# Performance work log

Hardware: AMD Instinct MI355X
Metric: run time of the kernel (lower is better)

Reference implementation:

```python
import jax, jax.numpy as jnp
import numpy as np

D_MODEL = 2048
FFN_MULT = 4
N_ROUTED = 8
TOP_K = 2
H_ROUTED = FFN_MULT * D_MODEL // N_ROUTED   # 1024
H_SHARED = FFN_MULT * D_MODEL               # 8192


def setup_inputs() -> dict:
    key = jax.random.key(0)
    ks = jax.random.split(key, 8)
    s = 0.02
    x = jax.random.normal(ks[0], (4, 2048, D_MODEL), dtype=jnp.float32)
    w_gate = jax.random.normal(ks[1], (N_ROUTED, D_MODEL), dtype=jnp.float32) * s
    Wg = jax.random.normal(ks[2], (N_ROUTED, D_MODEL, H_ROUTED), dtype=jnp.float32) * s
    Wu = jax.random.normal(ks[3], (N_ROUTED, D_MODEL, H_ROUTED), dtype=jnp.float32) * s
    Wd = jax.random.normal(ks[4], (N_ROUTED, H_ROUTED, D_MODEL), dtype=jnp.float32) * s
    Sg = jax.random.normal(ks[5], (D_MODEL, H_SHARED), dtype=jnp.float32) * s
    Su = jax.random.normal(ks[6], (D_MODEL, H_SHARED), dtype=jnp.float32) * s
    Sd = jax.random.normal(ks[7], (H_SHARED, D_MODEL), dtype=jnp.float32) * s
    return {"x": x, "w_gate": w_gate, "Wg": Wg, "Wu": Wu, "Wd": Wd,
            "Sg": Sg, "Su": Su, "Sd": Sd}


def reference(x, w_gate, Wg, Wu, Wd, Sg, Su, Sd):
    B, T, D = x.shape
    N = B * T
    xf = x.reshape(N, D)

    # shared expert (n_shared = 1)
    shared = (jax.nn.silu(xf @ Sg) * (xf @ Su)) @ Sd          # [N, D]

    # gate (eval mode: clean logits, no noise)
    clean = xf @ w_gate.T                                      # [N, E]
    top_logits, top_idx = jax.lax.top_k(clean, TOP_K)          # [N, K]
    gates = jax.nn.softmax(top_logits, axis=-1)                # [N, K]
    # load-balance loss
    importance = jax.nn.softmax(clean, axis=-1).sum(0)         # [E]
    ce = importance / N * N_ROUTED
    lb_loss = jnp.mean(ce * ce)

    # combine weights: combine[n,e] = sum_k gates[n,k] * (top_idx[n,k]==e)
    onehot = jax.nn.one_hot(top_idx, N_ROUTED, dtype=xf.dtype)  # [N, K, E]
    combine = jnp.einsum('nke,nk->ne', onehot, gates)           # [N, E]

    # routed experts (dense grouped form, zero-weight tokens contribute 0)
    hg = jnp.einsum('nd,edh->neh', xf, Wg)
    hu = jnp.einsum('nd,edh->neh', xf, Wu)
    h = jax.nn.silu(hg) * hu                                    # [N, E, H]
    routed = jnp.einsum('neh,ehd,ne->nd', h, Wd, combine)       # [N, D]

    out = (shared + routed).reshape(B, T, D)
    return out, lb_loss
```

## Files before the change

kernel.cpp:

```cpp
#include <hip/hip_runtime.h>
#include <hip/hip_bf16.h>
#include <hip/hip_fp16.h>
#include <stdint.h>

#define NTOK   8192
#define DM     2048
#define NEXP   8
#define HR     1024
#define HS     8192
#define ROWS_MAX 18432

typedef _Float16 f16;
typedef f16  f16x8 __attribute__((ext_vector_type(8)));
typedef float f32x4 __attribute__((ext_vector_type(4)));

#define GLP(p) ((const __attribute__((address_space(1))) void*)(p))
#define LDP(p) ((__attribute__((address_space(3))) void*)(p))

static __device__ __forceinline__ float silu_f(float v) {
  return v / (1.0f + __expf(-v));
}

static __device__ __forceinline__ int xcd_swz(int bid, int nwg) {
  const int q = nwg >> 3, r = nwg & 7;
  const int x = bid & 7, i = bid >> 3;
  return (x < r ? x * (q + 1) : r * (q + 1) + (x - r) * q) + i;
}


__global__ __launch_bounds__(256)
void conv_x_kernel(const float* __restrict__ in, f16* __restrict__ out, int n8) {
  const int i = blockIdx.x * 256 + threadIdx.x;
  if (i >= n8) return;
  const float4* p = (const float4*)in + (size_t)i * 2;
  const float4 a = p[0], b = p[1];
  f16x8 o;
  o[0] = (f16)a.x; o[1] = (f16)a.y; o[2] = (f16)a.z; o[3] = (f16)a.w;
  o[4] = (f16)b.x; o[5] = (f16)b.y; o[6] = (f16)b.z; o[7] = (f16)b.w;
  ((f16x8*)out)[i] = o;
}

__global__ __launch_bounds__(256)
void conv_t_kernel(const float* __restrict__ in, f16* __restrict__ out,
                   int R, int C, size_t ostride, int rmap) {
  __shared__ float t[32][33];
  const int b = blockIdx.z;
  const float* inb = in + (size_t)b * R * C;
  f16* outb = out + (size_t)b * ostride;
  const int c0 = blockIdx.x * 32, r0 = blockIdx.y * 32;
  const int tx = threadIdx.x, ty0 = threadIdx.y;
#pragma unroll
  for (int yy = 0; yy < 4; ++yy) {
    const int ty = ty0 + yy * 8;
    t[ty][tx] = inb[(size_t)(r0 + ty) * C + (c0 + tx)];
  }
  __syncthreads();
#pragma unroll
  for (int yy = 0; yy < 4; ++yy) {
    const int ty = ty0 + yy * 8;
    const int tr = c0 + ty;
    const int pr = rmap ? (((tr >> 4) << 5) + ((rmap - 1) << 4) + (tr & 15)) : tr;
    outb[(size_t)pr * R + (r0 + tx)] = (f16)t[tx][ty];
  }
}


__global__ __launch_bounds__(256)
void gate_kernel(const float* __restrict__ x, const float* __restrict__ wgate,
                 float* __restrict__ gateW, int* __restrict__ gateI,
                 float* __restrict__ importance, int* __restrict__ cnt) {
  __shared__ float impl[NEXP];
  __shared__ int cntl[NEXP];
  const int tid = threadIdx.x, lane = tid & 63, wid = tid >> 6;
  if (tid < NEXP) { impl[tid] = 0.f; cntl[tid] = 0; }
  __syncthreads();
  for (int s = 0; s < 8; ++s) {
    const int t = blockIdx.x * 32 + wid * 8 + s;
    const float* xr = x + (size_t)t * DM;
    float pv[NEXP] = {0.f, 0.f, 0.f, 0.f, 0.f, 0.f, 0.f, 0.f};
    for (int j = 0; j < DM / 64; ++j) {
      const int c = lane + j * 64;
      const float xv = xr[c];
#pragma unroll
      for (int e = 0; e < NEXP; ++e) pv[e] += xv * wgate[e * DM + c];
    }
#pragma unroll
    for (int e = 0; e < NEXP; ++e) {
#pragma unroll
      for (int st = 32; st >= 1; st >>= 1) pv[e] += __shfl_xor(pv[e], st);
    }
    if (lane == 0) {
      float v1 = pv[0]; int i1 = 0;
#pragma unroll
      for (int e = 1; e < NEXP; ++e) if (pv[e] > v1) { v1 = pv[e]; i1 = e; }
      float v2 = -1e30f; int i2 = 0;
#pragma unroll
      for (int e = 0; e < NEXP; ++e) if (e != i1 && pv[e] > v2) { v2 = pv[e]; i2 = e; }
      const float g1 = 1.f / (1.f + expf(v2 - v1));
      gateW[t * 2 + 0] = g1;  gateW[t * 2 + 1] = 1.f - g1;
      gateI[t * 2 + 0] = i1;  gateI[t * 2 + 1] = i2;
      float mx = pv[0];
#pragma unroll
      for (int e = 1; e < NEXP; ++e) mx = fmaxf(mx, pv[e]);
      float sum = 0.f, ex[NEXP];
#pragma unroll
      for (int e = 0; e < NEXP; ++e) { ex[e] = expf(pv[e] - mx); sum += ex[e]; }
      const float inv = 1.f / sum;
#pragma unroll
      for (int e = 0; e < NEXP; ++e) atomicAdd(&impl[e], ex[e] * inv);
      atomicAdd(&cntl[i1], 1);
      atomicAdd(&cntl[i2], 1);
    }
  }
  __syncthreads();
  if (tid < NEXP) {
    atomicAdd(&importance[tid], impl[tid]);
    atomicAdd(&cnt[tid], cntl[tid]);
  }
}

__global__ void scan_kernel(const int* __restrict__ cnt, int* __restrict__ seg,
                            int* __restrict__ cursor, const float* __restrict__ imp,
                            float* __restrict__ lb_out) {
  if (threadIdx.x == 0 && blockIdx.x == 0) {
    int o = 0;
#pragma unroll
    for (int e = 0; e < NEXP; ++e) {
      seg[e] = o;
      o += (cnt[e] + 255) & ~255;
      cursor[e] = 0;
    }
    seg[NEXP] = o;
    float s = 0.f;
#pragma unroll
    for (int e = 0; e < NEXP; ++e) {
      const float ce = imp[e] * ((float)NEXP / (float)NTOK);
      s += ce * ce;
    }
    *lb_out = s / (float)NEXP;
  }
}

__global__ __launch_bounds__(256)
void scatter_kernel(const float* __restrict__ gateW, const int* __restrict__ gateI,
                    const int* __restrict__ seg, int* __restrict__ cursor,
                    int* __restrict__ rowtok, float* __restrict__ rowgate) {
  const int t = blockIdx.x * 256 + threadIdx.x;
  const int lane = threadIdx.x & 63;
#pragma unroll
  for (int k = 0; k < 2; ++k) {
    const int e = gateI[t * 2 + k];
    const float g = gateW[t * 2 + k];
    for (int ee = 0; ee < NEXP; ++ee) {
      const unsigned long long m = __ballot(e == ee);
      if (e == ee) {
        const int leader = __ffsll((unsigned long long)m) - 1;
        const int rank = (int)__popcll(m & ((1ull << lane) - 1ull));
        int base = 0;
        if (lane == leader) base = atomicAdd(&cursor[ee], (int)__popcll(m));
        base = __shfl(base, leader);
        const int pos = seg[ee] + base + rank;
        rowtok[pos] = t;
        rowgate[pos] = g;
      }
    }
  }
}


struct G8Ptrs { const f16* a[4]; const f16* b[4]; };

static __device__ __forceinline__ void swz_rc(int tid, int i, int& r, int& c) {
  const int L = i * 8192 + tid * 16;
  const int U = L ^ (((L >> 7) & 7) << 4);
  r = U >> 7;
  c = (U & 127) >> 1;
}

static __device__ __forceinline__ void stage8(const G8Ptrs& P, int koff,
                                              f16* AsB, f16* BsB, int wid) {
#pragma unroll
  for (int i = 0; i < 4; ++i) {
    __builtin_amdgcn_global_load_lds(GLP(P.a[i] + koff), LDP(AsB + i * 4096 + wid * 512), 16, 0, 0);
    __builtin_amdgcn_global_load_lds(GLP(P.b[i] + koff), LDP(BsB + i * 4096 + wid * 512), 16, 0, 0);
  }
}

static __device__ __forceinline__ void g8_mainloop(const G8Ptrs& P, int nt,
                                                   f16* As, f16* Bs,
                                                   f32x4 (&acc)[8][4]) {
  const int tid = threadIdx.x;
  const int lane = tid & 63, wid = tid >> 6;
  const int wr = wid >> 2, wc = wid & 3;
  const int fr = lane & 15, fk = (lane >> 4) * 8;

  stage8(P, 0, As, Bs, wid);
  asm volatile("s_waitcnt vmcnt(0)" ::: "memory");
  __syncthreads();

  for (int t = 0; t < nt; ++t) {
    const int cur = t & 1;
    if (t + 1 < nt)
      stage8(P, (t + 1) * 64, As + (cur ^ 1) * 16384, Bs + (cur ^ 1) * 16384, wid);
    const f16* Ab = As + cur * 16384;
    const f16* Bb = Bs + cur * 16384;
    f16x8 bf[4][2];
#pragma unroll
    for (int n = 0; n < 4; ++n) {
      const int r = wc * 64 + n * 16 + fr;
      const int sw = (r & 7) << 3;
#pragma unroll
      for (int ks = 0; ks < 2; ++ks)
        bf[n][ks] = *(const f16x8*)&Bb[(r * 64 + ks * 32 + fk) ^ sw];
    }
#pragma unroll
    for (int mh = 0; mh < 2; ++mh) {
#pragma unroll
      for (int ks = 0; ks < 2; ++ks) {
        f16x8 af[4];
#pragma unroll
        for (int m = 0; m < 4; ++m) {
          const int r = wr * 128 + (mh * 4 + m) * 16 + fr;
          af[m] = *(const f16x8*)&Ab[(r * 64 + ks * 32 + fk) ^ ((r & 7) << 3)];
        }
#pragma unroll
        for (int m = 0; m < 4; ++m)
#pragma unroll
          for (int n = 0; n < 4; ++n)
            acc[mh * 4 + m][n] =
                __builtin_amdgcn_mfma_f32_16x16x32_f16(af[m], bf[n][ks], acc[mh * 4 + m][n], 0, 0, 0);
      }
    }
    asm volatile("s_waitcnt vmcnt(0)" ::: "memory");
    __syncthreads();
  }
}

__global__ __launch_bounds__(512, 2)
void g8_gu(const f16* __restrict__ A, const f16* __restrict__ B,
           f16* __restrict__ H, int gx, int Nh, int K) {
  __shared__ f16 As[2 * 16384], Bs[2 * 16384];
  const int lin = xcd_swz(blockIdx.x, gridDim.x);
  const int row0 = (lin % gx) * 256, n0 = (lin / gx) * 256;
  const int tid = threadIdx.x;
  G8Ptrs P;
#pragma unroll
  for (int i = 0; i < 4; ++i) {
    int r, c; swz_rc(tid, i, r, c);
    P.a[i] = A + (size_t)(row0 + r) * K + c;
    P.b[i] = B + (size_t)(n0 + r) * K + c;
  }
  f32x4 acc[8][4] = {};
  g8_mainloop(P, K / 64, As, Bs, acc);
  const int lane = tid & 63, wid = tid >> 6;
  const int wr = wid >> 2, wc = wid & 3;
  const int fr = lane & 15, r0 = (lane >> 4) * 4;
  const int hc0 = (n0 + wc * 64) >> 1;
#pragma unroll
  for (int m = 0; m < 8; ++m)
#pragma unroll
    for (int k = 0; k < 2; ++k)
#pragma unroll
      for (int rr = 0; rr < 4; ++rr) {
        const int row = row0 + wr * 128 + m * 16 + r0 + rr;
        const int hcol = hc0 + k * 16 + fr;
        const float g = acc[m][2 * k][rr];
        const float u = acc[m][2 * k + 1][rr];
        H[(size_t)row * Nh + hcol] = (f16)(silu_f(g) * u);
      }
}

__global__ __launch_bounds__(512, 2)
void g8_down(const f16* __restrict__ A, const f16* __restrict__ B,
             float* __restrict__ out, int gx, int N, int K) {
  __shared__ f16 As[2 * 16384], Bs[2 * 16384];
  const int lin = xcd_swz(blockIdx.x, gridDim.x);
  const int row0 = (lin % gx) * 256, n0 = (lin / gx) * 256;
  const int tid = threadIdx.x;
  G8Ptrs P;
#pragma unroll
  for (int i = 0; i < 4; ++i) {
    int r, c; swz_rc(tid, i, r, c);
    P.a[i] = A + (size_t)(row0 + r) * K + c;
    P.b[i] = B + (size_t)(n0 + r) * K + c;
  }
  f32x4 acc[8][4] = {};
  g8_mainloop(P, K / 64, As, Bs, acc);
  const int lane = tid & 63, wid = tid >> 6;
  const int wr = wid >> 2, wc = wid & 3;
  const int fr = lane & 15, r0 = (lane >> 4) * 4;
#pragma unroll
  for (int m = 0; m < 8; ++m)
#pragma unroll
    for (int n = 0; n < 4; ++n)
#pragma unroll
      for (int rr = 0; rr < 4; ++rr) {
        const int row = row0 + wr * 128 + m * 16 + r0 + rr;
        const int col = n0 + wc * 64 + n * 16 + fr;
        out[(size_t)row * N + col] = acc[m][n][rr];
      }
}

__global__ __launch_bounds__(512, 2)
void g8_rgu(const f16* __restrict__ x16, const int* __restrict__ rowtok,
            const f16* __restrict__ Wgu, f16* __restrict__ hr,
            const int* __restrict__ seg) {
  __shared__ f16 As[2 * 16384], Bs[2 * 16384];
  const int e = blockIdx.z;
  const int row0 = seg[e] + blockIdx.y * 256;
  if (row0 >= seg[e + 1]) return;
  const int n0 = blockIdx.x * 256;
  const f16* Bbase = Wgu + (size_t)e * 2048 * DM;
  const int tid = threadIdx.x;
  G8Ptrs P;
#pragma unroll
  for (int i = 0; i < 4; ++i) {
    int r, c; swz_rc(tid, i, r, c);
    int tok = rowtok[row0 + r];
    if (tok < 0) tok = 0;
    P.a[i] = x16 + (size_t)tok * DM + c;
    P.b[i] = Bbase + (size_t)(n0 + r) * DM + c;
  }
  f32x4 acc[8][4] = {};
  g8_mainloop(P, DM / 64, As, Bs, acc);
  const int lane = tid & 63, wid = tid >> 6;
  const int wr = wid >> 2, wc = wid & 3;
  const int fr = lane & 15, r0 = (lane >> 4) * 4;
  const int hc0 = (n0 + wc * 64) >> 1;
#pragma unroll
  for (int m = 0; m < 8; ++m)
#pragma unroll
    for (int k = 0; k < 2; ++k)
#pragma unroll
      for (int rr = 0; rr < 4; ++rr) {
        const int row = row0 + wr * 128 + m * 16 + r0 + rr;
        const int hcol = hc0 + k * 16 + fr;
        const float g = acc[m][2 * k][rr];
        const float u = acc[m][2 * k + 1][rr];
        hr[(size_t)row * HR + hcol] = (f16)(silu_f(g) * u);
      }
}

__global__ __launch_bounds__(512, 2)
void g8_rdown(const f16* __restrict__ A, const f16* __restrict__ B,
              float* __restrict__ out, const int* __restrict__ seg,
              const int* __restrict__ rowtok, const float* __restrict__ rowgate) {
  __shared__ f16 As[2 * 16384], Bs[2 * 16384];
  const int e = blockIdx.z;
  const int row0 = seg[e] + blockIdx.y * 256;
  if (row0 >= seg[e + 1]) return;
  const int n0 = blockIdx.x * 256;
  const f16* Bbase = B + (size_t)e * DM * HR;
  const int tid = threadIdx.x;
  G8Ptrs P;
#pragma unroll
  for (int i = 0; i < 4; ++i) {
    int r, c; swz_rc(tid, i, r, c);
    P.a[i] = A + (size_t)(row0 + r) * HR + c;
    P.b[i] = Bbase + (size_t)(n0 + r) * HR + c;
  }
  f32x4 acc[8][4] = {};
  g8_mainloop(P, HR / 64, As, Bs, acc);
  const int lane = tid & 63, wid = tid >> 6;
  const int wr = wid >> 2, wc = wid & 3;
  const int fr = lane & 15, r0 = (lane >> 4) * 4;
#pragma unroll
  for (int m = 0; m < 8; ++m)
#pragma unroll
    for (int rr = 0; rr < 4; ++rr) {
      const int pos = row0 + wr * 128 + m * 16 + r0 + rr;
      const int tok = rowtok[pos];
      if (tok >= 0) {
        const float gw = rowgate[pos];
#pragma unroll
        for (int n = 0; n < 4; ++n) {
          const int col = n0 + wc * 64 + n * 16 + fr;
          atomicAdd(&out[(size_t)tok * DM + col], acc[m][n][rr] * gw);
        }
      }
    }
}


extern "C" void kernel_launch(void* const* d_in, const int* in_sizes, int n_in,
                              void* d_out, int out_size, void* d_ws, size_t ws_size,
                              hipStream_t stream) {
  const float* x  = (const float*)d_in[0];
  const float* wg = (const float*)d_in[1];
  const float* Wg = (const float*)d_in[2];
  const float* Wu = (const float*)d_in[3];
  const float* Wd = (const float*)d_in[4];
  const float* Sg = (const float*)d_in[5];
  const float* Su = (const float*)d_in[6];
  const float* Sd = (const float*)d_in[7];
  float* out = (float*)d_out;

  char* p = (char*)d_ws;
  auto take = [&](size_t b) { char* q = p; p += (b + 255) & ~(size_t)255; return q; };
  float* importance = (float*)take(32);
  int*   cnt        = (int*)take(32);
  int*   cursor     = (int*)take(32);
  int*   seg        = (int*)take(64);
  int*   rowtok     = (int*)take((size_t)ROWS_MAX * 4);
  float* rowgate    = (float*)take((size_t)ROWS_MAX * 4);
  float* gateW      = (float*)take((size_t)NTOK * 2 * 4);
  int*   gateI      = (int*)take((size_t)NTOK * 2 * 4);
  f16* x16   = (f16*)take((size_t)NTOK * DM * 2);
  f16* SguI  = (f16*)take((size_t)2 * HS * DM * 2);
  f16* SdT   = (f16*)take((size_t)DM * HS * 2);
  f16* WguI  = (f16*)take((size_t)NEXP * 2048 * DM * 2);
  f16* WdT   = (f16*)take((size_t)NEXP * DM * HR * 2);
  f16* hbuf  = (f16*)take((size_t)NTOK * HS * 2);
  f16* hr    = (f16*)take((size_t)ROWS_MAX * HR * 2);
  if ((size_t)(p - (char*)d_ws) > ws_size) return;

  hipMemsetAsync(importance, 0, 768, stream);
  hipMemsetAsync(rowtok, 0xFF, (size_t)ROWS_MAX * 4, stream);

  conv_x_kernel<<<(NTOK * DM / 8 + 255) / 256, 256, 0, stream>>>(x, x16, NTOK * DM / 8);
  dim3 tb(32, 8);
  conv_t_kernel<<<dim3(HS / 32, DM / 32, 1), tb, 0, stream>>>(Sg, SguI, DM, HS, 0, 1);
  conv_t_kernel<<<dim3(HS / 32, DM / 32, 1), tb, 0, stream>>>(Su, SguI, DM, HS, 0, 2);
  conv_t_kernel<<<dim3(DM / 32, HS / 32, 1), tb, 0, stream>>>(Sd, SdT, HS, DM, 0, 0);
  conv_t_kernel<<<dim3(HR / 32, DM / 32, NEXP), tb, 0, stream>>>(Wg, WguI, DM, HR, (size_t)2048 * DM, 1);
  conv_t_kernel<<<dim3(HR / 32, DM / 32, NEXP), tb, 0, stream>>>(Wu, WguI, DM, HR, (size_t)2048 * DM, 2);
  conv_t_kernel<<<dim3(DM / 32, HR / 32, NEXP), tb, 0, stream>>>(Wd, WdT, HR, DM, (size_t)DM * HR, 0);

  gate_kernel<<<NTOK / 32, 256, 0, stream>>>(x, wg, gateW, gateI, importance, cnt);
  scan_kernel<<<1, 64, 0, stream>>>(cnt, seg, cursor, importance, out + (size_t)NTOK * DM);
  scatter_kernel<<<NTOK / 256, 256, 0, stream>>>(gateW, gateI, seg, cursor, rowtok, rowgate);

  g8_rgu<<<dim3(8, 64, NEXP), 512, 0, stream>>>(x16, rowtok, WguI, hr, seg);

  g8_gu<<<32 * 64, 512, 0, stream>>>(x16, SguI, hbuf, 32, HS, DM);
  g8_down<<<32 * 8, 512, 0, stream>>>(hbuf, SdT, out, 32, DM, HS);

  g8_rdown<<<dim3(8, 64, NEXP), 512, 0, stream>>>(hr, WdT, out, seg, rowtok, rowgate);
}
```

Baseline: 1.447 ms.

## Split GEMM mainloop into half-tile phases with finer prefetch waits; pre-gather routed rows

The shared GEMM mainloop now issues next-tile LDS prefetches in two halves around two barriers. It waits with partial vmcnt counts so the second half of the A tile loads while the first half of the MFMAs runs, rather than waiting for all loads at the end of each iteration. A new gather kernel copies routed token rows into a contiguous buffer (aliased onto hbuf, which is only written later), so the routed gate/up GEMM reads contiguous rows instead of indirecting through rowtok. This adds an extra memory pass and a launch. The hand-tuned waitcnt counts must exactly match the number of outstanding loads for correctness.

Measured after the change: 1.881 ms. 30.0% more time.

```diff
diff --git a/kernel.cpp b/kernel.cpp
--- a/kernel.cpp
+++ b/kernel.cpp
@@ -167,6 +167,19 @@
   }
 }
 
+__global__ __launch_bounds__(256)
+void gather_kernel(const f16* __restrict__ x16, const int* __restrict__ rowtok,
+                   f16* __restrict__ xg) {
+  const int row = blockIdx.x * 4 + (threadIdx.x >> 6);
+  const int lane = threadIdx.x & 63;
+  int tok = rowtok[row];
+  if (tok < 0) tok = 0;
+  const uint4* src = (const uint4*)(x16 + (size_t)tok * DM);
+  uint4* dst = (uint4*)(xg + (size_t)row * DM);
+#pragma unroll
+  for (int i = 0; i < 4; ++i) dst[lane + i * 64] = src[lane + i * 64];
+}
+
 
 struct G8Ptrs { const f16* a[4]; const f16* b[4]; };
 
@@ -175,15 +188,6 @@
   const int U = L ^ (((L >> 7) & 7) << 4);
   r = U >> 7;
   c = (U & 127) >> 1;
-}
-
-static __device__ __forceinline__ void stage8(const G8Ptrs& P, int koff,
-                                              f16* AsB, f16* BsB, int wid) {
-#pragma unroll
-  for (int i = 0; i < 4; ++i) {
-    __builtin_amdgcn_global_load_lds(GLP(P.a[i] + koff), LDP(AsB + i * 4096 + wid * 512), 16, 0, 0);
-    __builtin_amdgcn_global_load_lds(GLP(P.b[i] + koff), LDP(BsB + i * 4096 + wid * 512), 16, 0, 0);
-  }
 }
 
 static __device__ __forceinline__ void g8_mainloop(const G8Ptrs& P, int nt,
@@ -194,46 +198,76 @@
   const int wr = wid >> 2, wc = wid & 3;
   const int fr = lane & 15, fk = (lane >> 4) * 8;
 
-  stage8(P, 0, As, Bs, wid);
-  asm volatile("s_waitcnt vmcnt(0)" ::: "memory");
-  __syncthreads();
+#define STG_A(BUF, KOFF, U) \
+  __builtin_amdgcn_global_load_lds(GLP(P.a[U] + (KOFF)), LDP((BUF) + (U) * 4096 + wid * 512), 16, 0, 0)
+#define STG_B(BUF, KOFF, U) \
+  __builtin_amdgcn_global_load_lds(GLP(P.b[U] + (KOFF)), LDP((BUF) + (U) * 4096 + wid * 512), 16, 0, 0)
+
+  STG_B(Bs, 0, 0); STG_B(Bs, 0, 1); STG_B(Bs, 0, 2); STG_B(Bs, 0, 3);
+  STG_A(As, 0, 0); STG_A(As, 0, 2);
+  STG_A(As, 0, 1); STG_A(As, 0, 3);
 
   for (int t = 0; t < nt; ++t) {
     const int cur = t & 1;
-    if (t + 1 < nt)
-      stage8(P, (t + 1) * 64, As + (cur ^ 1) * 16384, Bs + (cur ^ 1) * 16384, wid);
     const f16* Ab = As + cur * 16384;
     const f16* Bb = Bs + cur * 16384;
+    f16* An = As + (cur ^ 1) * 16384;
+    f16* Bn = Bs + (cur ^ 1) * 16384;
+    const int koff = (t + 1) * 64;
+    const bool pf = (t + 1 < nt);
+
+    asm volatile("s_waitcnt vmcnt(2) lgkmcnt(0)" ::: "memory");
+    __builtin_amdgcn_s_barrier();
+    if (pf) {
+      STG_B(Bn, koff, 0); STG_B(Bn, koff, 1); STG_B(Bn, koff, 2); STG_B(Bn, koff, 3);
+      STG_A(An, koff, 0); STG_A(An, koff, 2);
+    }
     f16x8 bf[4][2];
 #pragma unroll
     for (int n = 0; n < 4; ++n) {
       const int r = wc * 64 + n * 16 + fr;
       const int sw = (r & 7) << 3;
-#pragma unroll
-      for (int ks = 0; ks < 2; ++ks)
-        bf[n][ks] = *(const f16x8*)&Bb[(r * 64 + ks * 32 + fk) ^ sw];
-    }
-#pragma unroll
-    for (int mh = 0; mh < 2; ++mh) {
-#pragma unroll
-      for (int ks = 0; ks < 2; ++ks) {
-        f16x8 af[4];
-#pragma unroll
-        for (int m = 0; m < 4; ++m) {
-          const int r = wr * 128 + (mh * 4 + m) * 16 + fr;
-          af[m] = *(const f16x8*)&Ab[(r * 64 + ks * 32 + fk) ^ ((r & 7) << 3)];
-        }
-#pragma unroll
-        for (int m = 0; m < 4; ++m)
-#pragma unroll
-          for (int n = 0; n < 4; ++n)
-            acc[mh * 4 + m][n] =
-                __builtin_amdgcn_mfma_f32_16x16x32_f16(af[m], bf[n][ks], acc[mh * 4 + m][n], 0, 0, 0);
-      }
-    }
-    asm volatile("s_waitcnt vmcnt(0)" ::: "memory");
-    __syncthreads();
-  }
+      bf[n][0] = *(const f16x8*)&Bb[(r * 64 + fk) ^ sw];
+      bf[n][1] = *(const f16x8*)&Bb[(r * 64 + 32 + fk) ^ sw];
+    }
+#pragma unroll
+    for (int ks = 0; ks < 2; ++ks) {
+      f16x8 af[4];
+#pragma unroll
+      for (int m = 0; m < 4; ++m) {
+        const int r = wr * 128 + m * 16 + fr;
+        af[m] = *(const f16x8*)&Ab[(r * 64 + ks * 32 + fk) ^ ((r & 7) << 3)];
+      }
+#pragma unroll
+      for (int m = 0; m < 4; ++m)
+#pragma unroll
+        for (int n = 0; n < 4; ++n)
+          acc[m][n] = __builtin_amdgcn_mfma_f32_16x16x32_f16(af[m], bf[n][ks], acc[m][n], 0, 0, 0);
+    }
+    if (pf) {
+      asm volatile("s_waitcnt vmcnt(6) lgkmcnt(0)" ::: "memory");
+    } else {
+      asm volatile("s_waitcnt vmcnt(0) lgkmcnt(0)" ::: "memory");
+    }
+    __builtin_amdgcn_s_barrier();
+    if (pf) { STG_A(An, koff, 1); STG_A(An, koff, 3); }
+#pragma unroll
+    for (int ks = 0; ks < 2; ++ks) {
+      f16x8 af[4];
+#pragma unroll
+      for (int m = 0; m < 4; ++m) {
+        const int r = wr * 128 + (4 + m) * 16 + fr;
+        af[m] = *(const f16x8*)&Ab[(r * 64 + ks * 32 + fk) ^ ((r & 7) << 3)];
+      }
+#pragma unroll
+      for (int m = 0; m < 4; ++m)
+#pragma unroll
+        for (int n = 0; n < 4; ++n)
+          acc[4 + m][n] = __builtin_amdgcn_mfma_f32_16x16x32_f16(af[m], bf[n][ks], acc[4 + m][n], 0, 0, 0);
+    }
+  }
+#undef STG_A
+#undef STG_B
 }
 
 __global__ __launch_bounds__(512, 2)
@@ -302,9 +336,8 @@
 }
 
 __global__ __launch_bounds__(512, 2)
-void g8_rgu(const f16* __restrict__ x16, const int* __restrict__ rowtok,
-            const f16* __restrict__ Wgu, f16* __restrict__ hr,
-            const int* __restrict__ seg) {
+void g8_rgu(const f16* __restrict__ xg, const f16* __restrict__ Wgu,
+            f16* __restrict__ hr, const int* __restrict__ seg) {
   __shared__ f16 As[2 * 16384], Bs[2 * 16384];
   const int e = blockIdx.z;
   const int row0 = seg[e] + blockIdx.y * 256;
@@ -316,9 +349,7 @@
 #pragma unroll
   for (int i = 0; i < 4; ++i) {
     int r, c; swz_rc(tid, i, r, c);
-    int tok = rowtok[row0 + r];
-    if (tok < 0) tok = 0;
-    P.a[i] = x16 + (size_t)tok * DM + c;
+    P.a[i] = xg + (size_t)(row0 + r) * DM + c;
     P.b[i] = Bbase + (size_t)(n0 + r) * DM + c;
   }
   f32x4 acc[8][4] = {};
@@ -412,6 +443,7 @@
   f16* WdT   = (f16*)take((size_t)NEXP * DM * HR * 2);
   f16* hbuf  = (f16*)take((size_t)NTOK * HS * 2);
   f16* hr    = (f16*)take((size_t)ROWS_MAX * HR * 2);
+  f16* xg    = hbuf;
   if ((size_t)(p - (char*)d_ws) > ws_size) return;
 
   hipMemsetAsync(importance, 0, 768, stream);
@@ -429,8 +461,9 @@
   gate_kernel<<<NTOK / 32, 256, 0, stream>>>(x, wg, gateW, gateI, importance, cnt);
   scan_kernel<<<1, 64, 0, stream>>>(cnt, seg, cursor, importance, out + (size_t)NTOK * DM);
   scatter_kernel<<<NTOK / 256, 256, 0, stream>>>(gateW, gateI, seg, cursor, rowtok, rowgate);
-
-  g8_rgu<<<dim3(8, 64, NEXP), 512, 0, stream>>>(x16, rowtok, WguI, hr, seg);
+  gather_kernel<<<ROWS_MAX / 4, 256, 0, stream>>>(x16, rowtok, xg);
+
+  g8_rgu<<<dim3(8, 64, NEXP), 512, 0, stream>>>(xg, WguI, hr, seg);
 
   g8_gu<<<32 * 64, 512, 0, stream>>>(x16, SguI, hbuf, 32, HS, DM);
   g8_down<<<32 * 8, 512, 0, stream>>>(hbuf, SdT, out, 32, DM, HS);
```

## Merge shared and routed expert GEMMs into single combined launches

Applied to the files above, without the earlier changes.

Folds the routed gate/up GEMM into the shared gate/up launch and the routed down GEMM into the shared down launch. Routed blocks are indexed over flattened row tiles, and each block finds its expert with a lookup over the segment offsets. The point is to fill the GPU better: the shared down GEMM alone launches only 256 large blocks, so routed work can run beside it, and the tails of the separate launches overlap. In exchange, the shared down output must now be written with atomic adds into an output buffer zeroed by an added memset, which costs extra memory traffic and atomic overhead.

Result: slower. 1.685 ms (+16.5%).

```diff
diff --git a/kernel.cpp b/kernel.cpp
--- a/kernel.cpp
+++ b/kernel.cpp
@@ -9,6 +9,7 @@
 #define HR     1024
 #define HS     8192
 #define ROWS_MAX 18432
+#define YT_MAX 72
 
 typedef _Float16 f16;
 typedef f16  f16x8 __attribute__((ext_vector_type(8)));
@@ -236,25 +237,56 @@
   }
 }
 
+static __device__ __forceinline__ int seg_lookup(const int* __restrict__ seg, int r0) {
+  int e = 0;
+#pragma unroll
+  for (int k = 1; k < NEXP; ++k) if (r0 >= seg[k]) e = k;
+  return e;
+}
+
 __global__ __launch_bounds__(512, 2)
-void g8_gu(const f16* __restrict__ A, const f16* __restrict__ B,
-           f16* __restrict__ H, int gx, int Nh, int K) {
+void g8_gu_all(const f16* __restrict__ x16, const f16* __restrict__ SguI,
+               f16* __restrict__ hbuf, const f16* __restrict__ Wgu,
+               f16* __restrict__ hr, const int* __restrict__ rowtok,
+               const int* __restrict__ seg) {
   __shared__ f16 As[2 * 16384], Bs[2 * 16384];
-  const int lin = xcd_swz(blockIdx.x, gridDim.x);
-  const int row0 = (lin % gx) * 256, n0 = (lin / gx) * 256;
   const int tid = threadIdx.x;
   G8Ptrs P;
-#pragma unroll
-  for (int i = 0; i < 4; ++i) {
-    int r, c; swz_rc(tid, i, r, c);
-    P.a[i] = A + (size_t)(row0 + r) * K + c;
-    P.b[i] = B + (size_t)(n0 + r) * K + c;
+  f16* H;
+  int Nh, row0, n0;
+  if (blockIdx.x < 2048) {
+    const int lin = xcd_swz(blockIdx.x, 2048);
+    row0 = (lin & 31) * 256;
+    n0 = (lin >> 5) * 256;
+#pragma unroll
+    for (int i = 0; i < 4; ++i) {
+      int r, c; swz_rc(tid, i, r, c);
+      P.a[i] = x16 + (size_t)(row0 + r) * DM + c;
+      P.b[i] = SguI + (size_t)(n0 + r) * DM + c;
+    }
+    H = hbuf; Nh = HS;
+  } else {
+    const int rb = blockIdx.x - 2048;
+    n0 = (rb & 7) * 256;
+    row0 = (rb >> 3) * 256;
+    if (row0 >= seg[NEXP]) return;
+    const int e = seg_lookup(seg, row0);
+    const f16* Bbase = Wgu + (size_t)e * 2048 * DM;
+#pragma unroll
+    for (int i = 0; i < 4; ++i) {
+      int r, c; swz_rc(tid, i, r, c);
+      int tok = rowtok[row0 + r];
+      if (tok < 0) tok = 0;
+      P.a[i] = x16 + (size_t)tok * DM + c;
+      P.b[i] = Bbase + (size_t)(n0 + r) * DM + c;
+    }
+    H = hr; Nh = HR;
   }
   f32x4 acc[8][4] = {};
-  g8_mainloop(P, K / 64, As, Bs, acc);
+  g8_mainloop(P, DM / 64, As, Bs, acc);
   const int lane = tid & 63, wid = tid >> 6;
   const int wr = wid >> 2, wc = wid & 3;
-  const int fr = lane & 15, r0 = (lane >> 4) * 4;
+  const int fr = lane & 15, r0v = (lane >> 4) * 4;
   const int hc0 = (n0 + wc * 64) >> 1;
 #pragma unroll
   for (int m = 0; m < 8; ++m)
@@ -262,7 +294,7 @@
     for (int k = 0; k < 2; ++k)
 #pragma unroll
       for (int rr = 0; rr < 4; ++rr) {
-        const int row = row0 + wr * 128 + m * 16 + r0 + rr;
+        const int row = row0 + wr * 128 + m * 16 + r0v + rr;
         const int hcol = hc0 + k * 16 + fr;
         const float g = acc[m][2 * k][rr];
         const float u = acc[m][2 * k + 1][rr];
@@ -271,114 +303,74 @@
 }
 
 __global__ __launch_bounds__(512, 2)
-void g8_down(const f16* __restrict__ A, const f16* __restrict__ B,
-             float* __restrict__ out, int gx, int N, int K) {
+void g8_down_all(const f16* __restrict__ hbuf, const f16* __restrict__ SdT,
+                 const f16* __restrict__ hr, const f16* __restrict__ WdT,
+                 float* __restrict__ out, const int* __restrict__ seg,
+                 const int* __restrict__ rowtok, const float* __restrict__ rowgate) {
   __shared__ f16 As[2 * 16384], Bs[2 * 16384];
-  const int lin = xcd_swz(blockIdx.x, gridDim.x);
-  const int row0 = (lin % gx) * 256, n0 = (lin / gx) * 256;
   const int tid = threadIdx.x;
   G8Ptrs P;
-#pragma unroll
-  for (int i = 0; i < 4; ++i) {
-    int r, c; swz_rc(tid, i, r, c);
-    P.a[i] = A + (size_t)(row0 + r) * K + c;
-    P.b[i] = B + (size_t)(n0 + r) * K + c;
+  int row0, n0, nt;
+  bool routed;
+  if (blockIdx.x < 256) {
+    const int lin = xcd_swz(blockIdx.x, 256);
+    row0 = (lin & 31) * 256;
+    n0 = (lin >> 5) * 256;
+#pragma unroll
+    for (int i = 0; i < 4; ++i) {
+      int r, c; swz_rc(tid, i, r, c);
+      P.a[i] = hbuf + (size_t)(row0 + r) * HS + c;
+      P.b[i] = SdT + (size_t)(n0 + r) * HS + c;
+    }
+    nt = HS / 64; routed = false;
+  } else {
+    const int rb = blockIdx.x - 256;
+    n0 = (rb & 7) * 256;
+    row0 = (rb >> 3) * 256;
+    if (row0 >= seg[NEXP]) return;
+    const int e = seg_lookup(seg, row0);
+    const f16* Bbase = WdT + (size_t)e * DM * HR;
+#pragma unroll
+    for (int i = 0; i < 4; ++i) {
+      int r, c; swz_rc(tid, i, r, c);
+      P.a[i] = hr + (size_t)(row0 + r) * HR + c;
+      P.b[i] = Bbase + (size_t)(n0 + r) * HR + c;
+    }
+    nt = HR / 64; routed = true;
   }
   f32x4 acc[8][4] = {};
-  g8_mainloop(P, K / 64, As, Bs, acc);
+  g8_mainloop(P, nt, As, Bs, acc);
   const int lane = tid & 63, wid = tid >> 6;
   const int wr = wid >> 2, wc = wid & 3;
-  const int fr = lane & 15, r0 = (lane >> 4) * 4;
-#pragma unroll
-  for (int m = 0; m < 8; ++m)
-#pragma unroll
-    for (int n = 0; n < 4; ++n)
+  const int fr = lane & 15, r0v = (lane >> 4) * 4;
+  if (!routed) {
+#pragma unroll
+    for (int m = 0; m < 8; ++m)
+#pragma unroll
+      for (int n = 0; n < 4; ++n)
+#pragma unroll
+        for (int rr = 0; rr < 4; ++rr) {
+          const int row = row0 + wr * 128 + m * 16 + r0v + rr;
+          const int col = n0 + wc * 64 + n * 16 + fr;
+          atomicAdd(&out[(size_t)row * DM + col], acc[m][n][rr]);
+        }
+  } else {
+#pragma unroll
+    for (int m = 0; m < 8; ++m)
 #pragma unroll
       for (int rr = 0; rr < 4; ++rr) {
-        const int row = row0 + wr * 128 + m * 16 + r0 + rr;
-        const int col = n0 + wc * 64 + n * 16 + fr;
-        out[(size_t)row * N + col] = acc[m][n][rr];
-      }
-}
-
-__global__ __launch_bounds__(512, 2)
-void g8_rgu(const f16* __restrict__ x16, const int* __restrict__ rowtok,
-            const f16* __restrict__ Wgu, f16* __restrict__ hr,
-            const int* __restrict__ seg) {
-  __shared__ f16 As[2 * 16384], Bs[2 * 16384];
-  const int e = blockIdx.z;
-  const int row0 = seg[e] + blockIdx.y * 256;
-  if (row0 >= seg[e + 1]) return;
-  const int n0 = blockIdx.x * 256;
-  const f16* Bbase = Wgu + (size_t)e * 2048 * DM;
-  const int tid = threadIdx.x;
-  G8Ptrs P;
-#pragma unroll
-  for (int i = 0; i < 4; ++i) {
-    int r, c; swz_rc(tid, i, r, c);
-    int tok = rowtok[row0 + r];
-    if (tok < 0) tok = 0;
-    P.a[i] = x16 + (size_t)tok * DM + c;
-    P.b[i] = Bbase + (size_t)(n0 + r) * DM + c;
-  }
-  f32x4 acc[8][4] = {};
-  g8_mainloop(P, DM / 64, As, Bs, acc);
-  const int lane = tid & 63, wid = tid >> 6;
-  const int wr = wid >> 2, wc = wid & 3;
-  const int fr = lane & 15, r0 = (lane >> 4) * 4;
-  const int hc0 = (n0 + wc * 64) >> 1;
-#pragma unroll
-  for (int m = 0; m < 8; ++m)
-#pragma unroll
-    for (int k = 0; k < 2; ++k)
-#pragma unroll
-      for (int rr = 0; rr < 4; ++rr) {
-        const int row = row0 + wr * 128 + m * 16 + r0 + rr;
-        const int hcol = hc0 + k * 16 + fr;
-        const float g = acc[m][2 * k][rr];
-        const float u = acc[m][2 * k + 1][rr];
-        hr[(size_t)row * HR + hcol] = (f16)(silu_f(g) * u);
-      }
-}
-
-__global__ __launch_bounds__(512, 2)
-void g8_rdown(const f16* __restrict__ A, const f16* __restrict__ B,
-              float* __restrict__ out, const int* __restrict__ seg,
-              const int* __restrict__ rowtok, const float* __restrict__ rowgate) {
-  __shared__ f16 As[2 * 16384], Bs[2 * 16384];
-  const int e = blockIdx.z;
-  const int row0 = seg[e] + blockIdx.y * 256;
-  if (row0 >= seg[e + 1]) return;
-  const int n0 = blockIdx.x * 256;
-  const f16* Bbase = B + (size_t)e * DM * HR;
-  const int tid = threadIdx.x;
-  G8Ptrs P;
-#pragma unroll
-  for (int i = 0; i < 4; ++i) {
-    int r, c; swz_rc(tid, i, r, c);
-    P.a[i] = A + (size_t)(row0 + r) * HR + c;
-    P.b[i] = Bbase + (size_t)(n0 + r) * HR + c;
-  }
-  f32x4 acc[8][4] = {};
-  g8_mainloop(P, HR / 64, As, Bs, acc);
-  const int lane = tid & 63, wid = tid >> 6;
-  const int wr = wid >> 2, wc = wid & 3;
-  const int fr = lane & 15, r0 = (lane >> 4) * 4;
-#pragma unroll
-  for (int m = 0; m < 8; ++m)
-#pragma unroll
-    for (int rr = 0; rr < 4; ++rr) {
-      const int pos = row0 + wr * 128 + m * 16 + r0 + rr;
-      const int tok = rowtok[pos];
-      if (tok >= 0) {
-        const float gw = rowgate[pos];
-#pragma unroll
-        for (int n = 0; n < 4; ++n) {
-          const int col = n0 + wc * 64 + n * 16 + fr;
-          atomicAdd(&out[(size_t)tok * DM + col], acc[m][n][rr] * gw);
+        const int pos = row0 + wr * 128 + m * 16 + r0v + rr;
+        const int tok = rowtok[pos];
+        if (tok >= 0) {
+          const float gw = rowgate[pos];
+#pragma unroll
+          for (int n = 0; n < 4; ++n) {
+            const int col = n0 + wc * 64 + n * 16 + fr;
+            atomicAdd(&out[(size_t)tok * DM + col], acc[m][n][rr] * gw);
+          }
         }
       }
-    }
+  }
 }
 
 
@@ -414,6 +406,7 @@
   f16* hr    = (f16*)take((size_t)ROWS_MAX * HR * 2);
   if ((size_t)(p - (char*)d_ws) > ws_size) return;
 
+  hipMemsetAsync(out, 0, (size_t)out_size * 4, stream);
   hipMemsetAsync(importance, 0, 768, stream);
   hipMemsetAsync(rowtok, 0xFF, (size_t)ROWS_MAX * 4, stream);
 
@@ -430,10 +423,7 @@
   scan_kernel<<<1, 64, 0, stream>>>(cnt, seg, cursor, importance, out + (size_t)NTOK * DM);
   scatter_kernel<<<NTOK / 256, 256, 0, stream>>>(gateW, gateI, seg, cursor, rowtok, rowgate);
 
-  g8_rgu<<<dim3(8, 64, NEXP), 512, 0, stream>>>(x16, rowtok, WguI, hr, seg);
-
-  g8_gu<<<32 * 64, 512, 0, stream>>>(x16, SguI, hbuf, 32, HS, DM);
-  g8_down<<<32 * 8, 512, 0, stream>>>(hbuf, SdT, out, 32, DM, HS);
-
-  g8_rdown<<<dim3(8, 64, NEXP), 512, 0, stream>>>(hr, WdT, out, seg, rowtok, rowgate);
-}
+  g8_gu_all<<<2048 + 8 * YT_MAX, 512, 0, stream>>>(x16, SguI, hbuf, WguI, hr, rowtok, seg);
+
+  g8_down_all<<<256 + 8 * YT_MAX, 512, 0, stream>>>(hbuf, SdT, hr, WdT, out, seg, rowtok, rowgate);
+}
```

## Merge weight conversion launches, fold x fp16 cast into gate, shrink routed grids

Applied to the files above, without the earlier changes.

Merges the six transpose/convert launches into one flat-grid conv_all kernel. It also drops the separate x fp16 conversion kernel by writing x16 from inside the gate kernel, which already reads x. The routed expert grids shrink from 64 to 33 row-tiles per expert, which relies on per-expert row counts fitting in 33 tiles. This removes launch overhead and a full re-read of x, but the gate kernel now does scalar fp16 stores and the shrunk grid could drop rows if routing is unbalanced.

After: 1.414 ms. -2.3%, faster.

```diff
diff --git a/kernel.cpp b/kernel.cpp
--- a/kernel.cpp
+++ b/kernel.cpp
@@ -29,32 +29,42 @@
 
 
 __global__ __launch_bounds__(256)
-void conv_x_kernel(const float* __restrict__ in, f16* __restrict__ out, int n8) {
-  const int i = blockIdx.x * 256 + threadIdx.x;
-  if (i >= n8) return;
-  const float4* p = (const float4*)in + (size_t)i * 2;
-  const float4 a = p[0], b = p[1];
-  f16x8 o;
-  o[0] = (f16)a.x; o[1] = (f16)a.y; o[2] = (f16)a.z; o[3] = (f16)a.w;
-  o[4] = (f16)b.x; o[5] = (f16)b.y; o[6] = (f16)b.z; o[7] = (f16)b.w;
-  ((f16x8*)out)[i] = o;
-}
-
-__global__ __launch_bounds__(256)
-void conv_t_kernel(const float* __restrict__ in, f16* __restrict__ out,
-                   int R, int C, size_t ostride, int rmap) {
+void conv_all_kernel(const float* __restrict__ Sg, const float* __restrict__ Su,
+                     const float* __restrict__ Sd, const float* __restrict__ Wg,
+                     const float* __restrict__ Wu, const float* __restrict__ Wd,
+                     f16* __restrict__ SguI, f16* __restrict__ SdT,
+                     f16* __restrict__ WguI, f16* __restrict__ WdT) {
   __shared__ float t[32][33];
-  const int b = blockIdx.z;
-  const float* inb = in + (size_t)b * R * C;
-  f16* outb = out + (size_t)b * ostride;
-  const int c0 = blockIdx.x * 32, r0 = blockIdx.y * 32;
+  const int bid = blockIdx.x;
+  const int s = bid >> 14, rr = bid & 16383;
+  const float* in;
+  f16* outb;
+  int C, xbits, rmap;
+  int b = 0, tile = rr;
+  if (s >= 3) { b = rr >> 11; tile = rr & 2047; }
+  switch (s) {
+    case 0:  in = Sg; outb = SguI; C = HS; xbits = 8; rmap = 1; break;
+    case 1:  in = Su; outb = SguI; C = HS; xbits = 8; rmap = 2; break;
+    case 2:  in = Sd; outb = SdT;  C = DM; xbits = 6; rmap = 0; break;
+    case 3:  in = Wg + (size_t)b * DM * HR; outb = WguI + (size_t)b * 2048 * DM;
+             C = HR; xbits = 5; rmap = 1; break;
+    case 4:  in = Wu + (size_t)b * DM * HR; outb = WguI + (size_t)b * 2048 * DM;
+             C = HR; xbits = 5; rmap = 2; break;
+    default: in = Wd + (size_t)b * HR * DM; outb = WdT + (size_t)b * DM * HR;
+             C = DM; xbits = 6; rmap = 0; break;
+  }
+  const int c0 = (tile & ((1 << xbits) - 1)) << 5;
+  const int r0 = (tile >> xbits) << 5;
+  const int R_out = C;
   const int tx = threadIdx.x, ty0 = threadIdx.y;
 #pragma unroll
   for (int yy = 0; yy < 4; ++yy) {
     const int ty = ty0 + yy * 8;
-    t[ty][tx] = inb[(size_t)(r0 + ty) * C + (c0 + tx)];
+    t[ty][tx] = in[(size_t)(r0 + ty) * C + (c0 + tx)];
   }
   __syncthreads();
+  const int R = (s == 2) ? HS : ((s == 5) ? HR : DM);
+  (void)R_out;
 #pragma unroll
   for (int yy = 0; yy < 4; ++yy) {
     const int ty = ty0 + yy * 8;
@@ -67,8 +77,9 @@
 
 __global__ __launch_bounds__(256)
 void gate_kernel(const float* __restrict__ x, const float* __restrict__ wgate,
-                 float* __restrict__ gateW, int* __restrict__ gateI,
-                 float* __restrict__ importance, int* __restrict__ cnt) {
+                 f16* __restrict__ x16, float* __restrict__ gateW,
+                 int* __restrict__ gateI, float* __restrict__ importance,
+                 int* __restrict__ cnt) {
   __shared__ float impl[NEXP];
   __shared__ int cntl[NEXP];
   const int tid = threadIdx.x, lane = tid & 63, wid = tid >> 6;
@@ -77,10 +88,12 @@
   for (int s = 0; s < 8; ++s) {
     const int t = blockIdx.x * 32 + wid * 8 + s;
     const float* xr = x + (size_t)t * DM;
+    f16* x16r = x16 + (size_t)t * DM;
     float pv[NEXP] = {0.f, 0.f, 0.f, 0.f, 0.f, 0.f, 0.f, 0.f};
     for (int j = 0; j < DM / 64; ++j) {
       const int c = lane + j * 64;
       const float xv = xr[c];
+      x16r[c] = (f16)xv;
 #pragma unroll
       for (int e = 0; e < NEXP; ++e) pv[e] += xv * wgate[e * DM + c];
     }
@@ -417,23 +430,17 @@
   hipMemsetAsync(importance, 0, 768, stream);
   hipMemsetAsync(rowtok, 0xFF, (size_t)ROWS_MAX * 4, stream);
 
-  conv_x_kernel<<<(NTOK * DM / 8 + 255) / 256, 256, 0, stream>>>(x, x16, NTOK * DM / 8);
-  dim3 tb(32, 8);
-  conv_t_kernel<<<dim3(HS / 32, DM / 32, 1), tb, 0, stream>>>(Sg, SguI, DM, HS, 0, 1);
-  conv_t_kernel<<<dim3(HS / 32, DM / 32, 1), tb, 0, stream>>>(Su, SguI, DM, HS, 0, 2);
-  conv_t_kernel<<<dim3(DM / 32, HS / 32, 1), tb, 0, stream>>>(Sd, SdT, HS, DM, 0, 0);
-  conv_t_kernel<<<dim3(HR / 32, DM / 32, NEXP), tb, 0, stream>>>(Wg, WguI, DM, HR, (size_t)2048 * DM, 1);
-  conv_t_kernel<<<dim3(HR / 32, DM / 32, NEXP), tb, 0, stream>>>(Wu, WguI, DM, HR, (size_t)2048 * DM, 2);
-  conv_t_kernel<<<dim3(DM / 32, HR / 32, NEXP), tb, 0, stream>>>(Wd, WdT, HR, DM, (size_t)DM * HR, 0);
-
-  gate_kernel<<<NTOK / 32, 256, 0, stream>>>(x, wg, gateW, gateI, importance, cnt);
+  gate_kernel<<<NTOK / 32, 256, 0, stream>>>(x, wg, x16, gateW, gateI, importance, cnt);
   scan_kernel<<<1, 64, 0, stream>>>(cnt, seg, cursor, importance, out + (size_t)NTOK * DM);
   scatter_kernel<<<NTOK / 256, 256, 0, stream>>>(gateW, gateI, seg, cursor, rowtok, rowgate);
 
-  g8_rgu<<<dim3(8, 64, NEXP), 512, 0, stream>>>(x16, rowtok, WguI, hr, seg);
+  conv_all_kernel<<<6 * 16384, dim3(32, 8), 0, stream>>>(Sg, Su, Sd, Wg, Wu, Wd,
+                                                         SguI, SdT, WguI, WdT);
+
+  g8_rgu<<<dim3(8, 33, NEXP), 512, 0, stream>>>(x16, rowtok, WguI, hr, seg);
 
   g8_gu<<<32 * 64, 512, 0, stream>>>(x16, SguI, hbuf, 32, HS, DM);
   g8_down<<<32 * 8, 512, 0, stream>>>(hbuf, SdT, out, 32, DM, HS);
 
-  g8_rdown<<<dim3(8, 64, NEXP), 512, 0, stream>>>(hr, WdT, out, seg, rowtok, rowgate);
-}
+  g8_rdown<<<dim3(8, 33, NEXP), 512, 0, stream>>>(hr, WdT, out, seg, rowtok, rowgate);
+}
```
